# Kernel tuning notes

Measured on AMD Instinct MI355X. Metric: run time of the kernel, lower is better.

The kernel has to match this reference:

```python
import jax, jax.numpy as jnp
import numpy as np

B, C, T_TEXT, T_FEAT = 32, 256, 512, 2048
DELTA = 0.1  # self.temperature


def setup_inputs() -> dict:
    key = jax.random.key(0)
    k1, k2 = jax.random.split(key)
    x = jax.random.normal(k1, (B, C, T_TEXT), dtype=jnp.float32)
    # token durations in frames, ~U[0, 8): avg ~4 frames/token -> T_FEAT ~ 2048
    w = jax.random.uniform(k2, (B, T_TEXT), dtype=jnp.float32) * 8.0
    x_mask = jnp.ones((B, T_TEXT), dtype=bool)
    y_mask = jnp.ones((B, T_FEAT), dtype=bool)
    return {"x": x, "w": w, "x_mask": x_mask, "y_mask": y_mask}


def reference(x, w, x_mask, y_mask):
    # Gaussian upsampling (arXiv 2010.04301) with fixed temperature DELTA.
    # x: (B, C, T_text), w: (B, T_text), x_mask: (B, T_text), y_mask: (B, T_feat)
    T_feats = y_mask.shape[-1]
    # frame time indices, zeroed where y_mask is False
    t = jnp.arange(T_feats, dtype=jnp.float32)[None, :] * y_mask.astype(jnp.float32)  # (B, T_feat)
    # Gaussian centers: cumulative duration minus half of own duration
    c = jnp.cumsum(w, axis=-1) - 0.5 * w  # (B, T_text)
    # energy: -delta * (t - c)^2  -> (B, T_feat, T_text)
    energy = -DELTA * (t[:, :, None] - c[:, None, :]) ** 2
    # mask out padded text tokens
    energy = jnp.where(x_mask[:, None, :], energy, -jnp.inf)
    p_attn = jax.nn.softmax(energy, axis=-1)  # (B, T_feat, T_text)
    # weighted sum over text tokens: (B, C, T_feat)
    out = jnp.einsum("btn,bcn->bct", p_attn, x)
    return out
```

## Files before the change

### kernel.cpp

```cpp
#include <hip/hip_runtime.h>
#include <hip/hip_bf16.h>

#define B_    32
#define C_    256
#define NT    512
#define TFEAT 2048
#define TT    32
#define UW    96
#define PRE   32
#define DELTA 0.1f
#define PSTR  104
#define XSTR  520
#define OSTR  516

#define PHAT_ELEMS ((size_t)B_ * 64 * TT * UW)
#define WS_NEED (PHAT_ELEMS * 2 + (size_t)B_ * 64 * 4)

typedef __attribute__((ext_vector_type(4))) float f32x4;
typedef __attribute__((ext_vector_type(8))) unsigned short u16x8;
typedef __attribute__((ext_vector_type(8))) __bf16 bf16x8;

static __device__ inline unsigned short f2bfbits(float f) {
    __bf16 h = (__bf16)f;
    return __builtin_bit_cast(unsigned short, h);
}
static __device__ inline float bf2f(unsigned short h) {
    return __uint_as_float(((unsigned)h) << 16);
}

__global__ __launch_bounds__(256, 2) void p_kernel(const float* __restrict__ w,
                                                   unsigned short* __restrict__ phat,
                                                   int* __restrict__ lotab) {
    __shared__ float cs[NT];
    __shared__ float wsum[8];
    __shared__ unsigned short Pt[TT][PSTR];
    __shared__ int sLO[4];

    int tid  = threadIdx.x;
    int bx   = blockIdx.x;
    int b    = bx & 31;
    int tg   = bx >> 5;
    int lane = tid & 63;
    int wv   = tid >> 6;

    float v0 = w[b * NT + tid];
    float v1 = w[b * NT + 256 + tid];
    float s0 = v0, s1 = v1;
#pragma unroll
    for (int off = 1; off < 64; off <<= 1) {
        float t0 = __shfl_up(s0, off);
        float t1 = __shfl_up(s1, off);
        if (lane >= off) { s0 += t0; s1 += t1; }
    }
    if (lane == 63) { wsum[wv] = s0; wsum[4 + wv] = s1; }
    __syncthreads();
    float pre0 = 0.f;
    float pre1 = wsum[0] + wsum[1] + wsum[2] + wsum[3];
#pragma unroll
    for (int i = 0; i < 4; ++i) if (i < wv) pre0 += wsum[i];
#pragma unroll
    for (int i = 0; i < 4; ++i) if (i < wv) pre1 += wsum[4 + i];
    cs[tid]       = pre0 + s0 - 0.5f * v0;
    cs[256 + tid] = pre1 + s1 - 0.5f * v1;
    __syncthreads();

    if (wv == 0) {
        int gid = lane >> 4;
        int k   = lane & 15;
        float ft = (float)((tg * 4 + gid) * TT);
        bool p = cs[32 * k + 31] < ft;
        unsigned long long m = __ballot(p);
        int K = __popcll((m >> (gid * 16)) & 0xFFFFull);
        int n;
        if (K >= 16) {
            n = NT;
        } else {
            int base = 32 * K;
            bool pa = cs[base + k] < ft;
            bool pb = cs[base + 16 + k] < ft;
            unsigned long long ma = __ballot(pa);
            unsigned long long mb = __ballot(pb);
            n = base + __popcll((ma >> (gid * 16)) & 0xFFFFull)
                     + __popcll((mb >> (gid * 16)) & 0xFFFFull);
        }
        if (k == 0) {
            int n1 = n < NT - 1 ? n : NT - 1;
            int n0 = n - 1 > 0 ? n - 1 : 0;
            int nstar = (fabsf(ft - cs[n0]) <= fabsf(ft - cs[n1])) ? n0 : n1;
            int L = (nstar - PRE) & ~3;
            if (L < 0) L = 0;
            if (L > NT - UW) L = NT - UW;
            sLO[gid] = L;
            lotab[b * 64 + tg * 4 + gid] = L;
        }
    }
    __syncthreads();

    int g = tid >> 3, j = tid & 7;

    for (int it = 0; it < 4; ++it) {
        int tile = tg * 4 + it;
        int LO = sLO[it];
        float ft = (float)(tile * TT + g);
        float e[12];
        float mx = -1e30f;
#pragma unroll
        for (int k = 0; k < 12; ++k) {
            float d = ft - cs[LO + j + 8 * k];
            e[k] = -DELTA * d * d;
            mx = fmaxf(mx, e[k]);
        }
        mx = fmaxf(mx, __shfl_xor(mx, 1));
        mx = fmaxf(mx, __shfl_xor(mx, 2));
        mx = fmaxf(mx, __shfl_xor(mx, 4));
        float p[12];
        float sum = 0.f;
#pragma unroll
        for (int k = 0; k < 12; ++k) {
            p[k] = __expf(e[k] - mx);
            sum += p[k];
        }
        sum += __shfl_xor(sum, 1);
        sum += __shfl_xor(sum, 2);
        sum += __shfl_xor(sum, 4);
        float inv = 1.f / fmaxf(sum, 1e-30f);
#pragma unroll
        for (int k = 0; k < 12; ++k)
            Pt[g][j + 8 * k] = f2bfbits(p[k] * inv);
        __syncthreads();

        const unsigned* pw = (const unsigned*)&Pt[0][0];
        unsigned* gd = (unsigned*)phat + (size_t)(b * 64 + tile) * 1536 + tid * 6;
        int a = tid >> 3, r6 = tid & 7;
#pragma unroll
        for (int q = 0; q < 6; ++q)
            gd[q] = pw[a * (PSTR / 2) + r6 * 6 + q];
        __syncthreads();
    }
}

__global__ __launch_bounds__(256, 2) void g_kernel(const float* __restrict__ x,
                                                   const unsigned short* __restrict__ phat,
                                                   const int* __restrict__ lotab,
                                                   float* __restrict__ out) {
    __shared__ unsigned short xs[16][XSTR];
    __shared__ float outbuf[16][OSTR];

    int tid  = threadIdx.x;
    int bx   = blockIdx.x;
    int b    = bx & 31;
    int cg   = bx >> 5;
    int c0   = cg * 16;
    int lane = tid & 63;
    int w    = tid >> 6;

    {
        int c = tid >> 4, k = tid & 15;
        const float* xr = x + ((size_t)(b * C_ + c0 + c)) * NT + k * 32;
#pragma unroll
        for (int jj = 0; jj < 4; ++jj) {
            f32x4 a0 = *reinterpret_cast<const f32x4*>(xr + jj * 8);
            f32x4 a1 = *reinterpret_cast<const f32x4*>(xr + jj * 8 + 4);
            bf16x8 vv;
#pragma unroll
            for (int q = 0; q < 4; ++q) {
                vv[q]     = (__bf16)a0[q];
                vv[q + 4] = (__bf16)a1[q];
            }
            *reinterpret_cast<bf16x8*>(&xs[c][k * 32 + jj * 8]) = vv;
        }
    }
    __syncthreads();

    int cc = lane & 15;
    int kg = lane >> 4;

    for (int s = 0; s < 16; ++s) {
        int tile = s * 4 + w;
        int LO = lotab[b * 64 + tile];

        const unsigned short* ap = phat + (size_t)(b * 64 + tile) * (TT * UW);
        bf16x8 af[2][3];
#pragma unroll
        for (int mt = 0; mt < 2; ++mt)
#pragma unroll
            for (int ks = 0; ks < 3; ++ks)
                af[mt][ks] = __builtin_bit_cast(bf16x8,
                    *reinterpret_cast<const u16x8*>(
                        ap + (mt * 16 + cc) * UW + ks * 32 + kg * 8));

        bf16x8 bfg[3];
#pragma unroll
        for (int ks = 0; ks < 3; ++ks)
            bfg[ks] = __builtin_bit_cast(bf16x8,
                *reinterpret_cast<const u16x8*>(&xs[cc][LO + ks * 32 + kg * 8]));

        f32x4 acc[2];
        acc[0] = (f32x4){0.f, 0.f, 0.f, 0.f};
        acc[1] = (f32x4){0.f, 0.f, 0.f, 0.f};
#pragma unroll
        for (int mt = 0; mt < 2; ++mt)
#pragma unroll
            for (int ks = 0; ks < 3; ++ks)
                acc[mt] = __builtin_amdgcn_mfma_f32_16x16x32_bf16(
                    af[mt][ks], bfg[ks], acc[mt], 0, 0, 0);

        int toff = (s & 3) * 128 + w * 32 + kg * 4;
#pragma unroll
        for (int mt = 0; mt < 2; ++mt)
            *reinterpret_cast<f32x4*>(&outbuf[cc][toff + mt * 16]) = acc[mt];

        if ((s & 3) == 3) {
            __syncthreads();
            int row = tid >> 4, kk = tid & 15;
            int tb = (s >> 2) * 512;
            float* ob = out + ((size_t)(b * C_ + c0 + row)) * TFEAT + tb;
#pragma unroll
            for (int jj = 0; jj < 8; ++jj) {
                f32x4 v = *reinterpret_cast<const f32x4*>(&outbuf[row][(kk + 16 * jj) * 4]);
                __builtin_nontemporal_store(v,
                    reinterpret_cast<f32x4*>(ob + (kk + 16 * jj) * 4));
            }
            __syncthreads();
        }
    }
}

#define TPB   2
#define NGRP  32
#define TSTR  36

__global__ __launch_bounds__(256, 2) void fused_fallback(const float* __restrict__ x,
                                                         const float* __restrict__ w,
                                                         float* __restrict__ out) {
    __shared__ float cs[NT];
    __shared__ float wsum[8];
    __shared__ unsigned short Pt[TT][PSTR];
    __shared__ float Sinv[TT];
    __shared__ int sLO[TPB];
    __shared__ float trans[4][16][TSTR];

    int tid  = threadIdx.x;
    int bx   = blockIdx.x;
    int b    = bx & 31;
    int grp  = bx >> 5;
    int lane = tid & 63;
    int wv   = tid >> 6;

    float v0 = w[b * NT + tid];
    float v1 = w[b * NT + 256 + tid];
    float s0 = v0, s1 = v1;
#pragma unroll
    for (int off = 1; off < 64; off <<= 1) {
        float t0 = __shfl_up(s0, off);
        float t1 = __shfl_up(s1, off);
        if (lane >= off) { s0 += t0; s1 += t1; }
    }
    if (lane == 63) { wsum[wv] = s0; wsum[4 + wv] = s1; }
    __syncthreads();
    float pre0 = 0.f;
    float pre1 = wsum[0] + wsum[1] + wsum[2] + wsum[3];
#pragma unroll
    for (int i = 0; i < 4; ++i) if (i < wv) pre0 += wsum[i];
#pragma unroll
    for (int i = 0; i < 4; ++i) if (i < wv) pre1 += wsum[4 + i];
    cs[tid]       = pre0 + s0 - 0.5f * v0;
    cs[256 + tid] = pre1 + s1 - 0.5f * v1;
    __syncthreads();

    if (wv == 0) {
        int gid = lane >> 4;
        int k   = lane & 15;
        if (gid < TPB) {
            float ft = (float)((grp * TPB + gid) * TT);
            bool p = cs[32 * k + 31] < ft;
            unsigned long long m = __ballot(p);
            int K = __popcll((m >> (gid * 16)) & 0xFFFFull);
            int n;
            if (K >= 16) {
                n = NT;
            } else {
                int base = 32 * K;
                bool pa = cs[base + k] < ft;
                bool pb = cs[base + 16 + k] < ft;
                unsigned long long ma = __ballot(pa);
                unsigned long long mb = __ballot(pb);
                n = base + __popcll((ma >> (gid * 16)) & 0xFFFFull)
                         + __popcll((mb >> (gid * 16)) & 0xFFFFull);
            }
            if (k == 0) {
                int n1 = n < NT - 1 ? n : NT - 1;
                int n0 = n - 1 > 0 ? n - 1 : 0;
                int nstar = (fabsf(ft - cs[n0]) <= fabsf(ft - cs[n1])) ? n0 : n1;
                int L = (nstar - PRE) & ~3;
                if (L < 0) L = 0;
                if (L > NT - UW) L = NT - UW;
                sLO[gid] = L;
            }
        }
    }
    __syncthreads();

    int g = tid >> 3, j = tid & 7;
    int arow = lane & 15, kg = lane >> 4;
    int rr = lane >> 3, tq = lane & 7;

    for (int it = 0; it < TPB; ++it) {
        {
            int LO = sLO[it];
            float ft = (float)((grp * TPB + it) * TT + g);
            float e[12];
            float mx = -1e30f;
#pragma unroll
            for (int k = 0; k < 12; ++k) {
                float d = ft - cs[LO + j + 8 * k];
                e[k] = -DELTA * d * d;
                mx = fmaxf(mx, e[k]);
            }
            mx = fmaxf(mx, __shfl_xor(mx, 1));
            mx = fmaxf(mx, __shfl_xor(mx, 2));
            mx = fmaxf(mx, __shfl_xor(mx, 4));
            float sum = 0.f;
#pragma unroll
            for (int k = 0; k < 12; ++k) {
                unsigned short pbv = f2bfbits(__expf(e[k] - mx));
                sum += bf2f(pbv);
                Pt[g][j + 8 * k] = pbv;
            }
            sum += __shfl_xor(sum, 1);
            sum += __shfl_xor(sum, 2);
            sum += __shfl_xor(sum, 4);
            if (j == 0) Sinv[g] = 1.f / fmaxf(sum, 1e-30f);
        }
        __syncthreads();

        int LO = sLO[it];
        bf16x8 pfrag[2][3];
#pragma unroll
        for (int tt = 0; tt < 2; ++tt)
#pragma unroll
            for (int ks = 0; ks < 3; ++ks)
                pfrag[tt][ks] = __builtin_bit_cast(bf16x8,
                    *reinterpret_cast<const u16x8*>(
                        &Pt[tt * 16 + arow][ks * 32 + kg * 8]));

        f32x4 acc[2][4];
#pragma unroll
        for (int tt = 0; tt < 2; ++tt)
#pragma unroll
            for (int m = 0; m < 4; ++m)
                acc[tt][m] = (f32x4){0.f, 0.f, 0.f, 0.f};

        const float* xb = x + ((size_t)b * C_) * NT + LO + kg * 8;
#pragma unroll
        for (int m = 0; m < 4; ++m) {
            const float* xr = xb + (size_t)(wv * 64 + m * 16 + arow) * NT;
            bf16x8 xf[3];
#pragma unroll
            for (int ks = 0; ks < 3; ++ks) {
                f32x4 a0 = *reinterpret_cast<const f32x4*>(xr + ks * 32);
                f32x4 a1 = *reinterpret_cast<const f32x4*>(xr + ks * 32 + 4);
                bf16x8 vv;
#pragma unroll
                for (int q = 0; q < 4; ++q) {
                    vv[q]     = (__bf16)a0[q];
                    vv[q + 4] = (__bf16)a1[q];
                }
                xf[ks] = vv;
            }
#pragma unroll
            for (int tt = 0; tt < 2; ++tt)
#pragma unroll
                for (int ks = 0; ks < 3; ++ks)
                    acc[tt][m] = __builtin_amdgcn_mfma_f32_16x16x32_bf16(
                        pfrag[tt][ks], xf[ks], acc[tt][m], 0, 0, 0);
        }

        int t0f = (grp * TPB + it) * TT;
        float* ob = out + ((size_t)b * C_) * TFEAT + t0f;
        f32x4 sv0 = *reinterpret_cast<const f32x4*>(&Sinv[kg * 4]);
        f32x4 sv1 = *reinterpret_cast<const f32x4*>(&Sinv[16 + kg * 4]);
#pragma unroll
        for (int m = 0; m < 4; ++m) {
            *reinterpret_cast<f32x4*>(&trans[wv][arow][kg * 4])      = acc[0][m] * sv0;
            *reinterpret_cast<f32x4*>(&trans[wv][arow][16 + kg * 4]) = acc[1][m] * sv1;
            f32x4 o0 = *reinterpret_cast<const f32x4*>(&trans[wv][rr][tq * 4]);
            f32x4 o1 = *reinterpret_cast<const f32x4*>(&trans[wv][8 + rr][tq * 4]);
            int cq = wv * 64 + m * 16;
            *reinterpret_cast<f32x4*>(ob + (size_t)(cq + rr) * TFEAT + tq * 4)     = o0;
            *reinterpret_cast<f32x4*>(ob + (size_t)(cq + 8 + rr) * TFEAT + tq * 4) = o1;
        }
        __syncthreads();
    }
}

extern "C" void kernel_launch(void* const* d_in, const int* in_sizes, int n_in,
                              void* d_out, int out_size, void* d_ws, size_t ws_size,
                              hipStream_t stream) {
    const float* x = (const float*)d_in[0];
    const float* w = (const float*)d_in[1];
    float* out = (float*)d_out;

    if (ws_size >= WS_NEED) {
        unsigned short* phat = (unsigned short*)d_ws;
        int* lotab = (int*)((char*)d_ws + PHAT_ELEMS * 2);
        hipLaunchKernelGGL(p_kernel, dim3(B_ * 16), dim3(256), 0, stream, w, phat, lotab);
        hipLaunchKernelGGL(g_kernel, dim3(B_ * 16), dim3(256), 0, stream,
                           x, phat, lotab, out);
    } else {
        hipLaunchKernelGGL(fused_fallback, dim3(B_ * NGRP), dim3(256), 0, stream,
                           x, w, out);
    }
}
```

Before: 39.14 us.

## Rewrite gather kernel with 512 threads and direct output stores without LDS staging

Replaces g_kernel with g2_kernel, which runs 8 waves per block and gives each wave 8 contiguous time tiles. MFMA accumulators are stored straight to global memory instead of being staged through a shared output buffer, which drops the outbuf LDS traffic and the barriers around it. The x load becomes a flat coalesced float4 load per thread, and the tile window start is aligned to 8 so the bf16x8 LDS reads stay aligned. The direct stores write only 16 bytes per lane per row, so global store coalescing may be worse than the previous staged 512-float row writes.

```diff
diff --git a/kernel.cpp b/kernel.cpp
--- a/kernel.cpp
+++ b/kernel.cpp
@@ -10,13 +10,14 @@
 #define PRE   32
 #define DELTA 0.1f
 #define PSTR  104
+#define CG    16
 #define XSTR  520
-#define OSTR  516
 
 #define PHAT_ELEMS ((size_t)B_ * 64 * TT * UW)
 #define WS_NEED (PHAT_ELEMS * 2 + (size_t)B_ * 64 * 4)
 
 typedef __attribute__((ext_vector_type(4))) float f32x4;
+typedef __attribute__((ext_vector_type(4))) __bf16 bf16x4;
 typedef __attribute__((ext_vector_type(8))) unsigned short u16x8;
 typedef __attribute__((ext_vector_type(8))) __bf16 bf16x8;
 
@@ -87,7 +88,7 @@
             int n1 = n < NT - 1 ? n : NT - 1;
             int n0 = n - 1 > 0 ? n - 1 : 0;
             int nstar = (fabsf(ft - cs[n0]) <= fabsf(ft - cs[n1])) ? n0 : n1;
-            int L = (nstar - PRE) & ~3;
+            int L = (nstar - PRE) & ~7;
             if (L < 0) L = 0;
             if (L > NT - UW) L = NT - UW;
             sLO[gid] = L;
@@ -139,90 +140,69 @@
     }
 }
 
-__global__ __launch_bounds__(256, 2) void g_kernel(const float* __restrict__ x,
-                                                   const unsigned short* __restrict__ phat,
-                                                   const int* __restrict__ lotab,
-                                                   float* __restrict__ out) {
-    __shared__ unsigned short xs[16][XSTR];
-    __shared__ float outbuf[16][OSTR];
+__global__ __launch_bounds__(512, 2) void g2_kernel(const float* __restrict__ x,
+                                                    const unsigned short* __restrict__ phat,
+                                                    const int* __restrict__ lotab,
+                                                    float* __restrict__ out) {
+    __shared__ __bf16 xsbf[CG][XSTR];
 
     int tid  = threadIdx.x;
     int bx   = blockIdx.x;
     int b    = bx & 31;
     int cg   = bx >> 5;
-    int c0   = cg * 16;
     int lane = tid & 63;
-    int w    = tid >> 6;
-
-    {
-        int c = tid >> 4, k = tid & 15;
-        const float* xr = x + ((size_t)(b * C_ + c0 + c)) * NT + k * 32;
-#pragma unroll
-        for (int jj = 0; jj < 4; ++jj) {
-            f32x4 a0 = *reinterpret_cast<const f32x4*>(xr + jj * 8);
-            f32x4 a1 = *reinterpret_cast<const f32x4*>(xr + jj * 8 + 4);
-            bf16x8 vv;
-#pragma unroll
-            for (int q = 0; q < 4; ++q) {
-                vv[q]     = (__bf16)a0[q];
-                vv[q + 4] = (__bf16)a1[q];
-            }
-            *reinterpret_cast<bf16x8*>(&xs[c][k * 32 + jj * 8]) = vv;
-        }
-    }
-    __syncthreads();
-
-    int cc = lane & 15;
+    int wv   = tid >> 6;
+
+    const float* xg = x + ((size_t)(b * C_ + cg * CG)) * NT;
+    f32x4 xr[4];
+#pragma unroll
+    for (int q = 0; q < 4; ++q)
+        xr[q] = *reinterpret_cast<const f32x4*>(xg + q * 2048 + tid * 4);
+#pragma unroll
+    for (int q = 0; q < 4; ++q) {
+        int f   = q * 2048 + tid * 4;
+        bf16x4 hv;
+#pragma unroll
+        for (int e = 0; e < 4; ++e) hv[e] = (__bf16)xr[q][e];
+        *reinterpret_cast<bf16x4*>(&xsbf[f >> 9][f & 511]) = hv;
+    }
+    __syncthreads();
+
+    int fr = lane & 15;
     int kg = lane >> 4;
-
-    for (int s = 0; s < 16; ++s) {
-        int tile = s * 4 + w;
-        int LO = lotab[b * 64 + tile];
-
-        const unsigned short* ap = phat + (size_t)(b * 64 + tile) * (TT * UW);
-        bf16x8 af[2][3];
-#pragma unroll
-        for (int mt = 0; mt < 2; ++mt)
-#pragma unroll
-            for (int ks = 0; ks < 3; ++ks)
-                af[mt][ks] = __builtin_bit_cast(bf16x8,
-                    *reinterpret_cast<const u16x8*>(
-                        ap + (mt * 16 + cc) * UW + ks * 32 + kg * 8));
-
-        bf16x8 bfg[3];
+    const unsigned short* pb = phat + (size_t)(b * 64) * (TT * UW);
+    const int* lt = lotab + b * 64;
+    float* ob = out + ((size_t)(b * C_ + cg * CG + fr)) * TFEAT + kg * 4;
+
+#pragma unroll 2
+    for (int i = 0; i < 8; ++i) {
+        int tile = wv * 8 + i;
+        int LO   = lt[tile];
+
+        const unsigned short* ap = pb + (size_t)tile * (TT * UW);
+        bf16x8 af0[3], af1[3], bfr[3];
+#pragma unroll
+        for (int ks = 0; ks < 3; ++ks) {
+            af0[ks] = __builtin_bit_cast(bf16x8,
+                *reinterpret_cast<const u16x8*>(ap + fr * UW + ks * 32 + kg * 8));
+            af1[ks] = __builtin_bit_cast(bf16x8,
+                *reinterpret_cast<const u16x8*>(ap + (16 + fr) * UW + ks * 32 + kg * 8));
+        }
 #pragma unroll
         for (int ks = 0; ks < 3; ++ks)
-            bfg[ks] = __builtin_bit_cast(bf16x8,
-                *reinterpret_cast<const u16x8*>(&xs[cc][LO + ks * 32 + kg * 8]));
-
-        f32x4 acc[2];
-        acc[0] = (f32x4){0.f, 0.f, 0.f, 0.f};
-        acc[1] = (f32x4){0.f, 0.f, 0.f, 0.f};
-#pragma unroll
-        for (int mt = 0; mt < 2; ++mt)
-#pragma unroll
-            for (int ks = 0; ks < 3; ++ks)
-                acc[mt] = __builtin_amdgcn_mfma_f32_16x16x32_bf16(
-                    af[mt][ks], bfg[ks], acc[mt], 0, 0, 0);
-
-        int toff = (s & 3) * 128 + w * 32 + kg * 4;
-#pragma unroll
-        for (int mt = 0; mt < 2; ++mt)
-            *reinterpret_cast<f32x4*>(&outbuf[cc][toff + mt * 16]) = acc[mt];
-
-        if ((s & 3) == 3) {
-            __syncthreads();
-            int row = tid >> 4, kk = tid & 15;
-            int tb = (s >> 2) * 512;
-            float* ob = out + ((size_t)(b * C_ + c0 + row)) * TFEAT + tb;
-#pragma unroll
-            for (int jj = 0; jj < 8; ++jj) {
-                f32x4 v = *reinterpret_cast<const f32x4*>(&outbuf[row][(kk + 16 * jj) * 4]);
-                __builtin_nontemporal_store(v,
-                    reinterpret_cast<f32x4*>(ob + (kk + 16 * jj) * 4));
-            }
-            __syncthreads();
-        }
+            bfr[ks] = *reinterpret_cast<const bf16x8*>(&xsbf[fr][LO + ks * 32 + kg * 8]);
+
+        f32x4 acc0 = (f32x4){0.f, 0.f, 0.f, 0.f};
+        f32x4 acc1 = (f32x4){0.f, 0.f, 0.f, 0.f};
+#pragma unroll
+        for (int ks = 0; ks < 3; ++ks) {
+            acc0 = __builtin_amdgcn_mfma_f32_16x16x32_bf16(af0[ks], bfr[ks], acc0, 0, 0, 0);
+            acc1 = __builtin_amdgcn_mfma_f32_16x16x32_bf16(af1[ks], bfr[ks], acc1, 0, 0, 0);
+        }
+
+        float* op = ob + (size_t)tile * TT;
+        __builtin_nontemporal_store(acc0, reinterpret_cast<f32x4*>(op));
+        __builtin_nontemporal_store(acc1, reinterpret_cast<f32x4*>(op + 16));
     }
 }
 
@@ -405,7 +385,7 @@
         unsigned short* phat = (unsigned short*)d_ws;
         int* lotab = (int*)((char*)d_ws + PHAT_ELEMS * 2);
         hipLaunchKernelGGL(p_kernel, dim3(B_ * 16), dim3(256), 0, stream, w, phat, lotab);
-        hipLaunchKernelGGL(g_kernel, dim3(B_ * 16), dim3(256), 0, stream,
+        hipLaunchKernelGGL(g2_kernel, dim3(B_ * CG), dim3(512), 0, stream,
                            x, phat, lotab, out);
     } else {
         hipLaunchKernelGGL(fused_fallback, dim3(B_ * NGRP), dim3(256), 0, stream,
```

Result: faster. 37.98 us (-3.0%).
